# Kernel tuning notes

Hardware: AMD Instinct MI355X
Metric: run time of the kernel (lower is better)

The kernel has to match this reference:

```python
import math
import jax, jax.numpy as jnp
from jax import lax
import numpy as np

D = 128            # head_dim
B = 16             # independent KV streams (e.g., heads)
S = 4096           # update sequence length
P = 4096           # reconstruction positions
MAX_SEQ_LEN = 8192
# (n_waves, ema_rate, freq_low, freq_high) per level, coarse -> fine
LEVELS = [(16, 0.001, 0.01, 1.0), (32, 0.005, 0.5, 3.0), (64, 0.02, 1.0, 6.0), (128, 0.05, 2.0, 10.0), (256, 0.1, 4.0, 20.0)]
TWO_PI = 2.0 * math.pi


def setup_inputs() -> dict:
    key = jax.random.key(0)
    ks = jax.random.split(key, 2 + len(LEVELS))
    inp = {}
    inp['kv_vectors'] = jax.random.normal(ks[0], (B, S, D), dtype=jnp.float32)
    inp['positions'] = jnp.arange(S, dtype=jnp.int32)
    inp['recon_positions'] = jnp.sort(jax.random.randint(ks[1], (P,), 0, MAX_SEQ_LEN, dtype=jnp.int32))
    for i, (n, a, lo, hi) in enumerate(LEVELS):
        k1, k2 = jax.random.split(ks[2 + i], 2)
        inp[f'W_enc_{i}'] = jax.random.normal(k1, (3 * n, D), dtype=jnp.float32) / math.sqrt(D)
        inp[f'W_dec_{i}'] = jax.random.normal(k2, (D, n), dtype=jnp.float32) / math.sqrt(n)
        inp[f'base_freqs_{i}'] = jnp.linspace(lo, hi, n, dtype=jnp.float32)
    return inp


def _ema_final(x, alpha):
    # x: [S, ...]; returns EMA state after S sequential steps from zero init.
    def step(c, xt):
        return (1.0 - alpha) * c + alpha * xt, None
    final, _ = lax.scan(step, jnp.zeros(x.shape[1:], x.dtype), x)
    return final


def _forward(kv_vectors, positions, recon_positions, params):
    pos_norm = positions.astype(jnp.float32)[:, None] / MAX_SEQ_LEN    # [S,1]
    rpos_norm = recon_positions.astype(jnp.float32)[:, None] / MAX_SEQ_LEN  # [P,1]
    out = jnp.zeros((kv_vectors.shape[0], recon_positions.shape[0], D), jnp.float32)
    for (n, alpha, _lo, _hi), (W_enc, W_dec, base_freqs) in zip(LEVELS, params):
        deltas = jnp.einsum('bsd,wd->bsw', kv_vectors, W_enc)          # [B,S,3n]
        d_freq, d_amp, d_phase = jnp.split(deltas, 3, axis=-1)         # each [B,S,n]
        pos_signal = jnp.sin(base_freqs[None, :] * pos_norm * TWO_PI)  # [S,n]
        xs = jnp.stack([d_freq * pos_signal[None], jnp.abs(d_amp), d_phase], axis=0)  # [3,B,S,n]
        xs = jnp.transpose(xs, (2, 0, 1, 3))                           # [S,3,B,n]
        freqs, amps, phases = _ema_final(xs, alpha)                    # each [B,n]
        wave_phases = TWO_PI * (freqs[:, None, :] + base_freqs[None, None, :]) * rpos_norm[None] + phases[:, None, :]
        wave_values = amps[:, None, :] * jnp.sin(wave_phases)          # [B,P,n]
        out = out + jnp.einsum('bpn,dn->bpd', wave_values, W_dec)
    return out


def reference(kv_vectors, positions, recon_positions,
              W_enc_0, W_dec_0, base_freqs_0,
              W_enc_1, W_dec_1, base_freqs_1,
              W_enc_2, W_dec_2, base_freqs_2,
              W_enc_3, W_dec_3, base_freqs_3,
              W_enc_4, W_dec_4, base_freqs_4):
    params = [(W_enc_0, W_dec_0, base_freqs_0), (W_enc_1, W_dec_1, base_freqs_1),
              (W_enc_2, W_dec_2, base_freqs_2), (W_enc_3, W_dec_3, base_freqs_3),
              (W_enc_4, W_dec_4, base_freqs_4)]
    return _forward(kv_vectors, positions, recon_positions, params)
```

## Files before the change

kernel.cpp:

```cpp
#include <hip/hip_runtime.h>

typedef __attribute__((ext_vector_type(8))) short short8;
typedef __attribute__((ext_vector_type(4))) float floatx4;

#define NLEV 5
#define B_   16
#define S_   4096
#define D_   128
#define P_   4096
#define CTOT 496
#define BP   (B_ * CTOT)
#define WPADG 512
#define CENC 1488
#define INV2PI 0.15915494309189535f
#define NJBLK 336

__device__ __forceinline__ unsigned short f2bf(float f) {
    unsigned u = __float_as_uint(f);
    u += 0x7fffu + ((u >> 16) & 1u);
    return (unsigned short)(u >> 16);
}
__device__ __forceinline__ unsigned int pack2(float a, float b) {
    return (unsigned int)f2bf(a) | ((unsigned int)f2bf(b) << 16);
}

__global__ void pack_weights(const float* __restrict__ we0, const float* __restrict__ we1,
                             const float* __restrict__ we2, const float* __restrict__ we3,
                             const float* __restrict__ we4,
                             const float* __restrict__ wd0, const float* __restrict__ wd1,
                             const float* __restrict__ wd2, const float* __restrict__ wd3,
                             const float* __restrict__ wd4,
                             unsigned short* __restrict__ wencb,
                             unsigned short* __restrict__ wdbT)
{
    int idx = blockIdx.x * 256 + threadIdx.x;
    const int NE = CENC * D_;
    if (idx < NE) {
        int c = idx >> 7, d = idx & 127;
        const float* src; int off;
        if (c < 48)        { src = we0; off = 0;   }
        else if (c < 144)  { src = we1; off = 48;  }
        else if (c < 336)  { src = we2; off = 144; }
        else               { src = (c < 720) ? we3 : we4; off = (c < 720) ? 336 : 720; }
        wencb[idx] = f2bf(src[(size_t)(c - off) * D_ + d]);
    } else {
        int k = idx - NE;
        if (k >= D_ * WPADG) return;
        int d = k >> 9, w = k & 511;
        float v = 0.0f;
        if (w < CTOT) {
            const float* src; int off, nl;
            if (w < 16)       { src = wd0; off = 0;   nl = 16;  }
            else if (w < 48)  { src = wd1; off = 16;  nl = 32;  }
            else if (w < 112) { src = wd2; off = 48;  nl = 64;  }
            else if (w < 240) { src = wd3; off = 112; nl = 128; }
            else              { src = wd4; off = 240; nl = 256; }
            v = src[(size_t)d * nl + (w - off)];
        }
        wdbT[k] = f2bf(v);
    }
}

__global__ __launch_bounds__(256) void encoder(
    const float* __restrict__ kv, const int* __restrict__ positions,
    const unsigned short* __restrict__ wencb,
    const float* __restrict__ bfr0, const float* __restrict__ bfr1,
    const float* __restrict__ bfr2, const float* __restrict__ bfr3,
    const float* __restrict__ bfr4,
    float* __restrict__ accb)
{
    __shared__ unsigned short kvb[64 * 136];
    __shared__ float pf[64];
    const int b   = blockIdx.y;
    const int bid = blockIdx.x;
    const int tid = threadIdx.x;

    int bx, lb;
    if (bid < 96)       { bx = bid / 24;            lb = bid % 24; }
    else if (bid < 144) { int r = bid - 96;  bx = 4 + r / 12; lb = r % 12; }
    else if (bid < 192) { int r = bid - 144; bx = 8 + r / 6;  lb = r % 6;  }
    else                { int r = bid - 192; bx = 16 + r / 3; lb = r % 3;  }
    const int t0 = S_ - 64 * (bx + 1);

    const float* src = kv + ((size_t)(b * S_ + t0)) * D_;
    #pragma unroll
    for (int f = 0; f < 8; ++f) {
        int idx = f * 256 + tid;
        int t = idx >> 5, d4 = idx & 31;
        float4 val = *(const float4*)(src + t * D_ + d4 * 4);
        unsigned long long u = (unsigned long long)pack2(val.x, val.y)
                             | ((unsigned long long)pack2(val.z, val.w) << 32);
        *(unsigned long long*)&kvb[t * 136 + d4 * 4] = u;
    }
    if (tid < 64) pf[tid] = (float)positions[t0 + tid] * (1.0f / 8192.0f);
    __syncthreads();

    const int wid = tid >> 6, lane = tid & 63, ln = lane & 15, quad = lane >> 4;

    const int cnt = 9 + (bx < 16 ? 12 : 0) + (bx < 8 ? 24 : 0) + (bx < 4 ? 48 : 0);
    int jid = lb * 4 + wid;
    if (jid >= cnt) return;

    const int   n_l[5]  = {16, 32, 64, 128, 256};
    const int   coff[5] = {0, 16, 48, 112, 240};
    const int   c3[5]   = {0, 48, 144, 336, 720};
    const float al[5]   = {0.001f, 0.005f, 0.02f, 0.05f, 0.1f};
    const float l2m[5]  = {-0.0014434169f, -0.0072315692f, -0.0291463449f,
                           -0.0740005794f, -0.1520030934f};
    const float* bfp[5] = {bfr0, bfr1, bfr2, bfr3, bfr4};

    int l = 0, ci = jid;
    {
        const int sz[5] = {3, 6, (bx < 16 ? 12 : 0), (bx < 8 ? 24 : 0), (bx < 4 ? 48 : 0)};
        #pragma unroll
        for (int q = 0; q < 4; ++q) {
            if (ci >= sz[l]) { ci -= sz[l]; ++l; }
        }
    }
    const int n = n_l[l];

    const unsigned short* wrow = wencb + (size_t)(c3[l] + ci * 16 + ln) * D_;
    floatx4 acc[4];
    #pragma unroll
    for (int m = 0; m < 4; ++m) acc[m] = (floatx4){0.f, 0.f, 0.f, 0.f};
    #pragma unroll
    for (int k = 0; k < 4; ++k) {
        short8 bfg = *(const short8*)(wrow + k * 32 + quad * 8);
        #pragma unroll
        for (int m = 0; m < 4; ++m) {
            short8 af = *(const short8*)&kvb[(m * 16 + ln) * 136 + k * 32 + quad * 8];
            acc[m] = __builtin_amdgcn_mfma_f32_16x16x32_bf16(af, bfg, acc[m], 0, 0, 0);
        }
    }

    const int kind  = (ci * 16) / n;
    const int local = ci * 16 + ln - kind * n;
    const float bsv = (kind == 0) ? bfp[l][local] : 0.0f;
    float s = 0.0f;
    #pragma unroll
    for (int m = 0; m < 4; ++m)
        #pragma unroll
        for (int r = 0; r < 4; ++r) {
            int   trel = m * 16 + quad * 4 + r;
            int   tg   = t0 + trel;
            float wt   = al[l] * exp2f((float)(S_ - 1 - tg) * l2m[l]);
            float v    = acc[m][r];
            if (kind == 0) {
                float rev = bsv * pf[trel];
                rev -= floorf(rev);
                v *= __builtin_amdgcn_sinf(rev);
            } else if (kind == 1) {
                v = fabsf(v);
            }
            s += wt * v;
        }
    s += __shfl_xor(s, 16);
    s += __shfl_xor(s, 32);
    if (lane < 16)
        atomicAdd(accb + (size_t)kind * BP + b * CTOT + coff[l] + local, s);
}

__global__ void combine(const float* __restrict__ accb,
                        float* __restrict__ parA, float* __restrict__ parQ,
                        float* __restrict__ parP,
                        const float* __restrict__ b0, const float* __restrict__ b1,
                        const float* __restrict__ b2, const float* __restrict__ b3,
                        const float* __restrict__ b4)
{
    int idx = blockIdx.x * 256 + threadIdx.x;
    if (idx >= B_ * WPADG) return;
    int b = idx >> 9, w = idx & 511;
    float A = 0.f, Q = 0.f, P = 0.f;
    if (w < CTOT) {
        const float* bf; int off;
        if (w < 16)       { bf = b0; off = 0;   }
        else if (w < 48)  { bf = b1; off = 16;  }
        else if (w < 112) { bf = b2; off = 48;  }
        else if (w < 240) { bf = b3; off = 112; }
        else              { bf = b4; off = 240; }
        float f  = accb[0 * BP + b * CTOT + w];
        A        = accb[1 * BP + b * CTOT + w];
        float ph = accb[2 * BP + b * CTOT + w];
        Q = f + bf[w - off];
        P = ph * INV2PI;
    }
    parA[idx] = A; parQ[idx] = Q; parP[idx] = P;
}

__global__ __launch_bounds__(256) void decoder(
    const float* __restrict__ parA, const float* __restrict__ parQ,
    const float* __restrict__ parP,
    const unsigned short* __restrict__ wdbT, const int* __restrict__ rpos,
    float* __restrict__ out)
{
    __shared__ unsigned short v[64 * 264];
    __shared__ float rpn[64];
    const int b = blockIdx.y, p0 = blockIdx.x * 64, tid = threadIdx.x;
    if (tid < 64) rpn[tid] = (float)rpos[p0 + tid] * (1.0f / 8192.0f);

    const int wid = tid >> 6, lane = tid & 63, ln = lane & 15, quad = lane >> 4;
    const int nt0 = wid * 2;

    floatx4 acc[4][2];
    #pragma unroll
    for (int m = 0; m < 4; ++m)
        #pragma unroll
        for (int j = 0; j < 2; ++j) acc[m][j] = (floatx4){0.f, 0.f, 0.f, 0.f};

    #pragma unroll
    for (int half = 0; half < 2; ++half) {
        const int w0 = half * 256;
        float Q  = parQ[b * WPADG + w0 + tid];
        float A  = parA[b * WPADG + w0 + tid];
        float Ph = parP[b * WPADG + w0 + tid];
        __syncthreads();
        for (int p = 0; p < 64; ++p) {
            float r = fmaf(Q, rpn[p], Ph);
            r -= floorf(r);
            v[p * 264 + tid] = f2bf(A * __builtin_amdgcn_sinf(r));
        }
        __syncthreads();

        #pragma unroll
        for (int kk = 0; kk < 8; ++kk) {
            short8 bn[2];
            #pragma unroll
            for (int j = 0; j < 2; ++j)
                bn[j] = *(const short8*)(wdbT + (size_t)((nt0 + j) * 16 + ln) * WPADG
                                         + w0 + kk * 32 + quad * 8);
            short8 am[4];
            #pragma unroll
            for (int m = 0; m < 4; ++m)
                am[m] = *(const short8*)&v[(m * 16 + ln) * 264 + kk * 32 + quad * 8];
            #pragma unroll
            for (int m = 0; m < 4; ++m)
                #pragma unroll
                for (int j = 0; j < 2; ++j)
                    acc[m][j] = __builtin_amdgcn_mfma_f32_16x16x32_bf16(
                                    am[m], bn[j], acc[m][j], 0, 0, 0);
        }
    }

    #pragma unroll
    for (int m = 0; m < 4; ++m)
        #pragma unroll
        for (int j = 0; j < 2; ++j)
            #pragma unroll
            for (int r = 0; r < 4; ++r) {
                int p = p0 + m * 16 + quad * 4 + r;
                int d = (nt0 + j) * 16 + ln;
                out[((size_t)(b * P_ + p)) * D_ + d] = acc[m][j][r];
            }
}

extern "C" void kernel_launch(void* const* d_in, const int* in_sizes, int n_in,
                              void* d_out, int out_size, void* d_ws, size_t ws_size,
                              hipStream_t stream)
{
    const float* kv        = (const float*)d_in[0];
    const int*   positions = (const int*)d_in[1];
    const int*   rpos      = (const int*)d_in[2];

    char* ws = (char*)d_ws;
    float*          accb  = (float*)(ws + 0);
    float*          parA  = (float*)(ws + 95232);
    float*          parQ  = (float*)(ws + 128000);
    float*          parP  = (float*)(ws + 160768);
    unsigned short* wencb = (unsigned short*)(ws + 193536);
    unsigned short* wdbT  = (unsigned short*)(ws + 574464);

    hipMemsetAsync(accb, 0, (size_t)(3 * BP) * sizeof(float), stream);

    pack_weights<<<1000, 256, 0, stream>>>(
        (const float*)d_in[3], (const float*)d_in[6], (const float*)d_in[9],
        (const float*)d_in[12], (const float*)d_in[15],
        (const float*)d_in[4], (const float*)d_in[7], (const float*)d_in[10],
        (const float*)d_in[13], (const float*)d_in[16],
        wencb, wdbT);

    encoder<<<dim3(NJBLK, B_), 256, 0, stream>>>(
        kv, positions, wencb,
        (const float*)d_in[5], (const float*)d_in[8], (const float*)d_in[11],
        (const float*)d_in[14], (const float*)d_in[17],
        accb);

    combine<<<(B_ * WPADG) / 256, 256, 0, stream>>>(
        accb, parA, parQ, parP,
        (const float*)d_in[5], (const float*)d_in[8], (const float*)d_in[11],
        (const float*)d_in[14], (const float*)d_in[17]);

    decoder<<<dim3(P_ / 64, B_), 256, 0, stream>>>(
        parA, parQ, parP, wdbT, rpos, (float*)d_out);
}
```

Before: 164.3 us.

## Fuse memset and combine into neighbors, strength-reduce EMA weights, pack bf16 converts

The accumulator memset moves into pack_weights, and the combine kernel is folded into the decoder's parameter load, which removes two launches. The encoder replaces a per-element exp2f for the EMA weight with incremental multiplies, which may add small rounding drift. Both kernels now use hardware fract, and the decoder converts pairs of values to bf16 with a single packed instruction. The decoder recomputes the combine logic in every block, which adds a small amount of redundant work.

Result: faster. 156.6 us (-4.7%).

```diff
diff --git a/kernel.cpp b/kernel.cpp
--- a/kernel.cpp
+++ b/kernel.cpp
@@ -31,9 +31,11 @@
                              const float* __restrict__ wd2, const float* __restrict__ wd3,
                              const float* __restrict__ wd4,
                              unsigned short* __restrict__ wencb,
-                             unsigned short* __restrict__ wdbT)
+                             unsigned short* __restrict__ wdbT,
+                             float* __restrict__ accb)
 {
     int idx = blockIdx.x * 256 + threadIdx.x;
+    if (idx < 3 * BP) accb[idx] = 0.0f;
     const int NE = CENC * D_;
     if (idx < NE) {
         int c = idx >> 7, d = idx & 127;
@@ -136,61 +138,46 @@
     const int kind  = (ci * 16) / n;
     const int local = ci * 16 + ln - kind * n;
     const float bsv = (kind == 0) ? bfp[l][local] : 0.0f;
+
+    const float l2 = l2m[l];
+    const float fs = exp2f(-l2);
+    const float fq = exp2f(-(float)(quad * 4) * l2);
+    const float em = exp2f(-16.0f * l2);
+    float fr[4];
+    fr[0] = fq; fr[1] = fq * fs; fr[2] = fr[1] * fs; fr[3] = fr[2] * fs;
+    float Cm = al[l] * exp2f((float)(S_ - 1 - t0) * l2);
+
     float s = 0.0f;
     #pragma unroll
-    for (int m = 0; m < 4; ++m)
+    for (int m = 0; m < 4; ++m) {
         #pragma unroll
         for (int r = 0; r < 4; ++r) {
             int   trel = m * 16 + quad * 4 + r;
-            int   tg   = t0 + trel;
-            float wt   = al[l] * exp2f((float)(S_ - 1 - tg) * l2m[l]);
+            float wt   = Cm * fr[r];
             float v    = acc[m][r];
             if (kind == 0) {
                 float rev = bsv * pf[trel];
-                rev -= floorf(rev);
+                rev = __builtin_amdgcn_fractf(rev);
                 v *= __builtin_amdgcn_sinf(rev);
             } else if (kind == 1) {
                 v = fabsf(v);
             }
             s += wt * v;
         }
+        Cm *= em;
+    }
     s += __shfl_xor(s, 16);
     s += __shfl_xor(s, 32);
     if (lane < 16)
         atomicAdd(accb + (size_t)kind * BP + b * CTOT + coff[l] + local, s);
 }
 
-__global__ void combine(const float* __restrict__ accb,
-                        float* __restrict__ parA, float* __restrict__ parQ,
-                        float* __restrict__ parP,
-                        const float* __restrict__ b0, const float* __restrict__ b1,
-                        const float* __restrict__ b2, const float* __restrict__ b3,
-                        const float* __restrict__ b4)
-{
-    int idx = blockIdx.x * 256 + threadIdx.x;
-    if (idx >= B_ * WPADG) return;
-    int b = idx >> 9, w = idx & 511;
-    float A = 0.f, Q = 0.f, P = 0.f;
-    if (w < CTOT) {
-        const float* bf; int off;
-        if (w < 16)       { bf = b0; off = 0;   }
-        else if (w < 48)  { bf = b1; off = 16;  }
-        else if (w < 112) { bf = b2; off = 48;  }
-        else if (w < 240) { bf = b3; off = 112; }
-        else              { bf = b4; off = 240; }
-        float f  = accb[0 * BP + b * CTOT + w];
-        A        = accb[1 * BP + b * CTOT + w];
-        float ph = accb[2 * BP + b * CTOT + w];
-        Q = f + bf[w - off];
-        P = ph * INV2PI;
-    }
-    parA[idx] = A; parQ[idx] = Q; parP[idx] = P;
-}
-
 __global__ __launch_bounds__(256) void decoder(
-    const float* __restrict__ parA, const float* __restrict__ parQ,
-    const float* __restrict__ parP,
+    const float* __restrict__ accb,
     const unsigned short* __restrict__ wdbT, const int* __restrict__ rpos,
+    const float* __restrict__ b0, const float* __restrict__ b1,
+    const float* __restrict__ b2, const float* __restrict__ b3,
+    const float* __restrict__ b4,
     float* __restrict__ out)
 {
     __shared__ unsigned short v[64 * 264];
@@ -210,14 +197,31 @@
     #pragma unroll
     for (int half = 0; half < 2; ++half) {
         const int w0 = half * 256;
-        float Q  = parQ[b * WPADG + w0 + tid];
-        float A  = parA[b * WPADG + w0 + tid];
-        float Ph = parP[b * WPADG + w0 + tid];
+        const int w = w0 + tid;
+        float A = 0.f, Q = 0.f, Ph = 0.f;
+        if (w < CTOT) {
+            const float* bf; int off;
+            if (w < 16)       { bf = b0; off = 0;   }
+            else if (w < 48)  { bf = b1; off = 16;  }
+            else if (w < 112) { bf = b2; off = 48;  }
+            else if (w < 240) { bf = b3; off = 112; }
+            else              { bf = b4; off = 240; }
+            float f  = accb[0 * BP + b * CTOT + w];
+            A        = accb[1 * BP + b * CTOT + w];
+            float ph = accb[2 * BP + b * CTOT + w];
+            Q  = f + bf[w - off];
+            Ph = ph * INV2PI;
+        }
         __syncthreads();
-        for (int p = 0; p < 64; ++p) {
-            float r = fmaf(Q, rpn[p], Ph);
-            r -= floorf(r);
-            v[p * 264 + tid] = f2bf(A * __builtin_amdgcn_sinf(r));
+        for (int p = 0; p < 64; p += 2) {
+            float r0 = __builtin_amdgcn_fractf(fmaf(Q, rpn[p],     Ph));
+            float r1 = __builtin_amdgcn_fractf(fmaf(Q, rpn[p + 1], Ph));
+            float s0 = A * __builtin_amdgcn_sinf(r0);
+            float s1 = A * __builtin_amdgcn_sinf(r1);
+            unsigned pk;
+            asm("v_cvt_pk_bf16_f32 %0, %1, %2" : "=v"(pk) : "v"(s0), "v"(s1));
+            v[p * 264 + tid]       = (unsigned short)pk;
+            v[(p + 1) * 264 + tid] = (unsigned short)(pk >> 16);
         }
         __syncthreads();
 
@@ -263,20 +267,15 @@
 
     char* ws = (char*)d_ws;
     float*          accb  = (float*)(ws + 0);
-    float*          parA  = (float*)(ws + 95232);
-    float*          parQ  = (float*)(ws + 128000);
-    float*          parP  = (float*)(ws + 160768);
-    unsigned short* wencb = (unsigned short*)(ws + 193536);
-    unsigned short* wdbT  = (unsigned short*)(ws + 574464);
-
-    hipMemsetAsync(accb, 0, (size_t)(3 * BP) * sizeof(float), stream);
+    unsigned short* wencb = (unsigned short*)(ws + 95232);
+    unsigned short* wdbT  = (unsigned short*)(ws + 476160);
 
     pack_weights<<<1000, 256, 0, stream>>>(
         (const float*)d_in[3], (const float*)d_in[6], (const float*)d_in[9],
         (const float*)d_in[12], (const float*)d_in[15],
         (const float*)d_in[4], (const float*)d_in[7], (const float*)d_in[10],
         (const float*)d_in[13], (const float*)d_in[16],
-        wencb, wdbT);
+        wencb, wdbT, accb);
 
     encoder<<<dim3(NJBLK, B_), 256, 0, stream>>>(
         kv, positions, wencb,
@@ -284,11 +283,9 @@
         (const float*)d_in[14], (const float*)d_in[17],
         accb);
 
-    combine<<<(B_ * WPADG) / 256, 256, 0, stream>>>(
-        accb, parA, parQ, parP,
+    decoder<<<dim3(P_ / 64, B_), 256, 0, stream>>>(
+        accb, wdbT, rpos,
         (const float*)d_in[5], (const float*)d_in[8], (const float*)d_in[11],
-        (const float*)d_in[14], (const float*)d_in[17]);
-
-    decoder<<<dim3(P_ / 64, B_), 256, 0, stream>>>(
-        parA, parQ, parP, wdbT, rpos, (float*)d_out);
-}
+        (const float*)d_in[14], (const float*)d_in[17],
+        (float*)d_out);
+}
```
